# Performance work log

Measured on AMD Instinct MI355X. Metric: run time of the kernel, lower is better.

The kernel has to match this reference:

```python
import jax, jax.numpy as jnp
import numpy as np

EPS = 1e-7  # dummy-column epsilon from stanza utils.add_dummy(eps=True)


def setup_inputs() -> dict:
    key = jax.random.key(0)
    ks = jax.random.split(key, 9)
    n_mentions, emb = 10000, 1024
    batch, n_ants, pw_emb = 1024, 64, 64
    hidden = 1024
    in_features = 3 * emb + pw_emb  # 3136
    return {
        "all_mentions": jax.random.normal(ks[0], (n_mentions, emb), jnp.float32),
        "mentions_batch": jax.random.normal(ks[1], (batch, emb), jnp.float32),
        "pw_batch": jax.random.normal(ks[2], (batch, n_ants, pw_emb), jnp.float32),
        "top_indices_batch": jax.random.randint(ks[3], (batch, n_ants), 0, n_mentions),
        "top_rough_scores_batch": jax.random.normal(ks[4], (batch, n_ants), jnp.float32),
        "W1": jax.random.normal(ks[5], (hidden, in_features), jnp.float32) * 0.02,
        "b1": jax.random.normal(ks[6], (hidden,), jnp.float32) * 0.02,
        "Wout": jax.random.normal(ks[7], (1, hidden), jnp.float32) * 0.02,
        "bout": jax.random.normal(ks[8], (1,), jnp.float32) * 0.02,
    }


def reference(all_mentions, mentions_batch, pw_batch, top_indices_batch,
              top_rough_scores_batch, W1, b1, Wout, bout):
    n_ants = pw_batch.shape[1]
    # pair matrix: [batch, n_ants, 3*emb + pw_emb]
    a = jnp.broadcast_to(mentions_batch[:, None, :],
                         (mentions_batch.shape[0], n_ants, mentions_batch.shape[1]))
    b = all_mentions[top_indices_batch]          # gather: [batch, n_ants, emb]
    pair = jnp.concatenate((a, b, a * b, pw_batch), axis=2)
    # FFNN: Linear -> LeakyReLU (dropout is identity at eval) -> Linear(->1)
    h = jax.nn.leaky_relu(jnp.einsum('bnf,hf->bnh', pair, W1) + b1, negative_slope=0.01)
    ffnn = (jnp.einsum('bnh,oh->bno', h, Wout) + bout)[..., 0]  # [batch, n_ants]
    scores = top_rough_scores_batch + ffnn
    # add dummy column with eps at position 0 -> [batch, n_ants + 1]
    dummy = jnp.full((scores.shape[0], 1), EPS, scores.dtype)
    return jnp.concatenate((dummy, scores), axis=1)
```

## Files before the change

kernel.cpp:

```cpp
#include <hip/hip_runtime.h>
#include <hip/hip_bf16.h>
#include <cstdint>
#include <cstdio>

typedef unsigned short u16;
typedef unsigned int   u32;
typedef __attribute__((ext_vector_type(8))) short bf16x8;
typedef __attribute__((ext_vector_type(4))) float f32x4;
typedef __attribute__((ext_vector_type(4))) u16   u16x4;
typedef __attribute__((ext_vector_type(8))) u16   u16x8;

#define GLOBAL_AS __attribute__((address_space(1)))
#define LDS_AS    __attribute__((address_space(3)))

static __device__ __forceinline__ u16 f2bf(float f) {
  u32 u = __builtin_bit_cast(u32, f);
  u = (u + 0x7fffu + ((u >> 16) & 1u)) >> 16;
  return (u16)u;
}
static __device__ __forceinline__ float bf2f(u16 v) {
  return __builtin_bit_cast(float, (u32)v << 16);
}
static __device__ __forceinline__ void gload_lds16(const void* g, void* l) {
  __builtin_amdgcn_global_load_lds((GLOBAL_AS u32*)g, (LDS_AS u32*)l, 16, 0, 0);
}

__global__ void k_cvt(const float* __restrict__ src, int ld, int c0,
                      int rows_src, int cols4, int total4,
                      u16* __restrict__ dst, int ldd, int dcol) {
  int gid = blockIdx.x * 256 + threadIdx.x;
  if (gid >= total4) return;
  int r = gid / cols4;
  int c = (gid - r * cols4) * 4;
  u16x4 o = {0, 0, 0, 0};
  if (r < rows_src) {
    const float4 v = *(const float4*)&src[(size_t)r * ld + c0 + c];
    o[0] = f2bf(v.x); o[1] = f2bf(v.y); o[2] = f2bf(v.z); o[3] = f2bf(v.w);
  }
  *(u16x4*)&dst[(size_t)r * ldd + dcol + c] = o;
}

__global__ void k_init(const float* __restrict__ rough,
                       const float* __restrict__ bout,
                       float* __restrict__ out) {
  int i = blockIdx.x * 256 + threadIdx.x;
  if (i >= 1024 * 65) return;
  int bi = i / 65, c = i - bi * 65;
  out[i] = (c == 0) ? 1e-7f : rough[bi * 64 + c - 1] + bout[0];
}

__global__ void k_build_cmat(const u16* __restrict__ A16,
                             const u16* __restrict__ allm16,
                             const float* __restrict__ pw,
                             const int* __restrict__ topidx,
                             u16* __restrict__ Cmat, int r0) {
  int gid = blockIdx.x * 256 + threadIdx.x;
  int lr = gid / 136;
  int c8 = gid - lr * 136;
  int r  = r0 + lr;
  u16x8 o;
  if (c8 < 128) {
    int k   = c8 * 8;
    int idx = topidx[r];
    int bi  = r >> 6;
    u16x8 a = *(const u16x8*)&A16[(size_t)bi * 1024 + k];
    u16x8 b = *(const u16x8*)&allm16[(size_t)idx * 1024 + k];
#pragma unroll
    for (int j = 0; j < 8; ++j) o[j] = f2bf(bf2f(a[j]) * bf2f(b[j]));
  } else {
    int k = (c8 - 128) * 8;
    float4 p0 = *(const float4*)&pw[(size_t)r * 64 + k];
    float4 p1 = *(const float4*)&pw[(size_t)r * 64 + k + 4];
    o[0] = f2bf(p0.x); o[1] = f2bf(p0.y); o[2] = f2bf(p0.z); o[3] = f2bf(p0.w);
    o[4] = f2bf(p1.x); o[5] = f2bf(p1.y); o[6] = f2bf(p1.z); o[7] = f2bf(p1.w);
  }
  *(u16x8*)&Cmat[(size_t)lr * 1088 + c8 * 8] = o;
}

__global__ __launch_bounds__(256)
void gemm128(const u16* __restrict__ A, int lda,
             const u16* __restrict__ B, int ldb, int Ksteps,
             u16* __restrict__ C, int ldc, const float* __restrict__ bias) {
  __shared__ u16 As[128 * 64];
  __shared__ u16 Bs[128 * 64];
  const int t = threadIdx.x;
  const int w = t >> 6, l = t & 63;
  const int wr = w >> 1, wc = w & 1;
  const int brow = blockIdx.x * 128;
  const int bcol = blockIdx.y * 128;
  const int srow = t >> 3;
  const int scol = (t & 7) * 8;
  const int gsw  = (((t & 7) ^ ((t >> 3) & 7))) * 8;

  f32x4 acc[4][4] = {};
  for (int ks = 0; ks < Ksteps; ++ks) {
    const int kb = ks * 64;
#pragma unroll
    for (int q = 0; q < 4; ++q) {
      int r = q * 32 + srow;
      gload_lds16(A + (size_t)(brow + r) * lda + kb + gsw, &As[r * 64 + scol]);
      gload_lds16(B + (size_t)(bcol + r) * ldb + kb + gsw, &Bs[r * 64 + scol]);
    }
    __syncthreads();
#pragma unroll
    for (int kk = 0; kk < 2; ++kk) {
      bf16x8 af[4], bfr[4];
      const int pg = ((kk * 4 + (l >> 4)) ^ (l & 7)) * 8;
#pragma unroll
      for (int m = 0; m < 4; ++m)
        af[m] = *(const bf16x8*)&As[(wr * 64 + m * 16 + (l & 15)) * 64 + pg];
#pragma unroll
      for (int n = 0; n < 4; ++n)
        bfr[n] = *(const bf16x8*)&Bs[(wc * 64 + n * 16 + (l & 15)) * 64 + pg];
#pragma unroll
      for (int m = 0; m < 4; ++m)
#pragma unroll
        for (int n = 0; n < 4; ++n)
          acc[m][n] = __builtin_amdgcn_mfma_f32_16x16x32_bf16(af[m], bfr[n], acc[m][n], 0, 0, 0);
    }
    __syncthreads();
  }
#pragma unroll
  for (int m = 0; m < 4; ++m)
#pragma unroll
    for (int n = 0; n < 4; ++n)
#pragma unroll
      for (int reg = 0; reg < 4; ++reg) {
        int row = brow + wr * 64 + m * 16 + (l >> 4) * 4 + reg;
        int col = bcol + wc * 64 + n * 16 + (l & 15);
        float v = acc[m][n][reg] + (bias ? bias[col] : 0.f);
        C[(size_t)row * ldc + col] = f2bf(v);
      }
}

template<bool FUSED>
__global__ __launch_bounds__(512, 1)
void gemm256(const u16* __restrict__ A, int lda,
             const u16* __restrict__ B, int ldb, int NT,
             u16* __restrict__ C, int ldc,
             const u16* __restrict__ Aproj, const u16* __restrict__ Bproj,
             const float* __restrict__ Wout,
             const int* __restrict__ topidx, float* __restrict__ out, int r0) {
  extern __shared__ u16 lds[];
  u16* As = lds;
  u16* Bs = lds + 2 * 2 * 128 * 64;

  const int t = threadIdx.x;
  const int l = t & 63;
  const int w = t >> 6;
  const int wrow = w >> 2, wcol = w & 3;
  const int brow = blockIdx.x * 256;
  const int bcol = blockIdx.y * 256;

  const int sr  = t >> 3;
  const int sc  = (t & 7) * 8;
  const int gsw = ((t & 7) ^ (sr & 7)) * 8;

  auto stageA = [&](int kt, int h) {
    if (kt >= NT) return;
#pragma unroll
    for (int s = 0; s < 2; ++s) {
      int lr = sr + 64 * s;
      int g  = ((lr >> 5) << 6) + h * 32 + (lr & 31);
      gload_lds16(A + (size_t)(brow + g) * lda + kt * 64 + gsw,
                  &As[(((kt & 1) * 2 + h) * 128 + lr) * 64 + sc]);
    }
  };
  auto stageB = [&](int kt, int h) {
    if (kt >= NT) return;
#pragma unroll
    for (int s = 0; s < 2; ++s) {
      int lr = h * 128 + sr + 64 * s;
      gload_lds16(B + (size_t)(bcol + lr) * ldb + kt * 64 + gsw,
                  &Bs[((kt & 1) * 256 + lr) * 64 + sc]);
    }
  };

  f32x4 acc[8][4] = {};

  stageB(0, 0); stageB(0, 1); stageA(0, 0); stageA(0, 1);
  stageB(1, 0); stageB(1, 1);
  asm volatile("s_waitcnt vmcnt(6)" ::: "memory");
  __builtin_amdgcn_s_barrier();

  for (int kt = 0; kt < NT; ++kt) {
    const int cbuf = kt & 1;
    bf16x8 bfr[4][2];
#pragma unroll
    for (int q = 0; q < 4; ++q) {
      if (q == 0) {
#pragma unroll
        for (int n = 0; n < 4; ++n) {
          int row = wcol * 64 + n * 16 + (l & 15);
#pragma unroll
          for (int kk = 0; kk < 2; ++kk) {
            int gran = (kk * 4 + (l >> 4)) ^ (l & 7);
            bfr[n][kk] = *(const bf16x8*)&Bs[(cbuf * 256 + row) * 64 + gran * 8];
          }
        }
      }
      bf16x8 af[2][2];
#pragma unroll
      for (int m2 = 0; m2 < 2; ++m2) {
        int m = 2 * q + m2;
        int g = wrow * 128 + m * 16 + (l & 15);
        int lra = ((g >> 6) << 5) + (g & 31);
#pragma unroll
        for (int kk = 0; kk < 2; ++kk) {
          int gran = (kk * 4 + (l >> 4)) ^ (l & 7);
          af[m2][kk] = *(const bf16x8*)&As[((cbuf * 2 + (q & 1)) * 128 + lra) * 64 + gran * 8];
        }
      }

      if      (q == 0) stageA(kt + 1, 0);
      else if (q == 1) stageA(kt + 1, 1);
      else if (q == 2) stageB(kt + 2, 0);
      else             stageB(kt + 2, 1);

      if (q == 0) asm volatile("s_waitcnt lgkmcnt(8)" ::: "memory");
      __builtin_amdgcn_s_barrier();
      asm volatile("s_waitcnt lgkmcnt(0)" ::: "memory");
      __builtin_amdgcn_sched_barrier(0);
      __builtin_amdgcn_s_setprio(1);
#pragma unroll
      for (int m2 = 0; m2 < 2; ++m2)
#pragma unroll
        for (int n = 0; n < 4; ++n)
#pragma unroll
          for (int kk = 0; kk < 2; ++kk)
            acc[2 * q + m2][n] = __builtin_amdgcn_mfma_f32_16x16x32_bf16(
                af[m2][kk], bfr[n][kk], acc[2 * q + m2][n], 0, 0, 0);
      __builtin_amdgcn_s_setprio(0);

      if (q == 0) {
        if (kt + 1 < NT) asm volatile("s_waitcnt vmcnt(6)" ::: "memory");
        else             asm volatile("s_waitcnt vmcnt(0)" ::: "memory");
      } else if (q == 3 && kt + 1 < NT) {
        if (kt + 2 < NT) asm volatile("s_waitcnt vmcnt(6)" ::: "memory");
        else             asm volatile("s_waitcnt vmcnt(2)" ::: "memory");
      }
      __builtin_amdgcn_s_barrier();
    }
  }

  if constexpr (FUSED) {
    __syncthreads();
    u16* Pb = lds;
#pragma unroll
    for (int pass = 0; pass < 16; ++pass) {
      int rr = pass * 16 + (t >> 5);
      int mi = topidx[r0 + brow + rr];
      int cc = (t & 31) * 8;
      gload_lds16(&Bproj[(size_t)mi * 1024 + bcol + cc], &Pb[rr * 256 + cc]);
    }
    asm volatile("s_waitcnt vmcnt(0)" ::: "memory");
    __syncthreads();

    float wo[4], av[2][4];
    const int bi0 = ((r0 + brow) >> 6) + wrow * 2;
#pragma unroll
    for (int n = 0; n < 4; ++n) {
      int col = bcol + wcol * 64 + n * 16 + (l & 15);
      wo[n] = Wout[col];
#pragma unroll
      for (int j = 0; j < 2; ++j)
        av[j][n] = bf2f(Aproj[(size_t)(bi0 + j) * 1024 + col]);
    }
#pragma unroll
    for (int m = 0; m < 8; ++m) {
#pragma unroll
      for (int reg = 0; reg < 4; ++reg) {
        int lrow = wrow * 128 + m * 16 + (l >> 4) * 4 + reg;
        int gr = r0 + brow + lrow;
        float s = 0.f;
#pragma unroll
        for (int n = 0; n < 4; ++n) {
          int lcol = wcol * 64 + n * 16 + (l & 15);
          float v = acc[m][n][reg] + av[m >> 2][n] + bf2f(Pb[lrow * 256 + lcol]);
          v = v > 0.f ? v : 0.01f * v;
          s += v * wo[n];
        }
        s += __shfl_xor(s, 1);
        s += __shfl_xor(s, 2);
        s += __shfl_xor(s, 4);
        s += __shfl_xor(s, 8);
        if ((l & 15) == 0)
          atomicAdd(&out[(gr >> 6) * 65 + 1 + (gr & 63)], s);
      }
    }
  } else {
#pragma unroll
    for (int m = 0; m < 8; ++m)
#pragma unroll
      for (int n = 0; n < 4; ++n)
#pragma unroll
        for (int reg = 0; reg < 4; ++reg) {
          int row = brow + wrow * 128 + m * 16 + (l >> 4) * 4 + reg;
          int col = bcol + wcol * 64 + n * 16 + (l & 15);
          C[(size_t)row * ldc + col] = f2bf(acc[m][n][reg]);
        }
  }
}

extern "C" void kernel_launch(void* const* d_in, const int* in_sizes, int n_in,
                              void* d_out, int out_size, void* d_ws, size_t ws_size,
                              hipStream_t stream) {
  const float* allm  = (const float*)d_in[0];
  const float* ments = (const float*)d_in[1];
  const float* pw    = (const float*)d_in[2];
  const int*   tidx  = (const int*)d_in[3];
  const float* rough = (const float*)d_in[4];
  const float* W1    = (const float*)d_in[5];
  const float* b1    = (const float*)d_in[6];
  const float* Wout  = (const float*)d_in[7];
  const float* bout  = (const float*)d_in[8];
  float* out = (float*)d_out;

  const int CHUNK = 16384;
  u16* A16    = (u16*)d_ws;
  u16* allm16 = A16 + 1024 * 1024;
  u16* W1a    = allm16 + 10240 * 1024;
  u16* W1b    = W1a + 1024 * 1024;
  u16* W1cp   = W1b + 1024 * 1024;
  u16* Aproj  = W1cp + 1024 * 1088;
  u16* Bproj  = Aproj + 1024 * 1024;
  u16* Cmat   = Bproj + 10240 * 1024;

  size_t need = (size_t)2 * ((size_t)1024*1024 + 10240*1024 + 1024*1024 + 1024*1024
              + 1024*1088 + 1024*1024 + 10240*1024 + (size_t)CHUNK*1088);
  if (ws_size < need) {
    fprintf(stderr, "kernel_launch: ws_size %zu < needed %zu\n", ws_size, need);
    return;
  }

  hipFuncSetAttribute((const void*)&gemm256<false>,
                      hipFuncAttributeMaxDynamicSharedMemorySize, 131072);
  hipFuncSetAttribute((const void*)&gemm256<true>,
                      hipFuncAttributeMaxDynamicSharedMemorySize, 131072);

  {
    int t4;
    t4 = 1024 * 256;
    k_cvt<<<(t4 + 255) / 256, 256, 0, stream>>>(W1, 3136, 0,    1024, 256, t4, W1a, 1024, 0);
    k_cvt<<<(t4 + 255) / 256, 256, 0, stream>>>(W1, 3136, 1024, 1024, 256, t4, W1b, 1024, 0);
    k_cvt<<<(t4 + 255) / 256, 256, 0, stream>>>(W1, 3136, 2048, 1024, 256, t4, W1cp, 1088, 0);
    t4 = 1024 * 16;
    k_cvt<<<(t4 + 255) / 256, 256, 0, stream>>>(W1, 3136, 3072, 1024, 16, t4, W1cp, 1088, 1024);
    t4 = 1024 * 256;
    k_cvt<<<(t4 + 255) / 256, 256, 0, stream>>>(ments, 1024, 0, 1024, 256, t4, A16, 1024, 0);
    t4 = 10240 * 256;
    k_cvt<<<(t4 + 255) / 256, 256, 0, stream>>>(allm, 1024, 0, 10000, 256, t4, allm16, 1024, 0);
  }

  gemm128<<<dim3(8, 8), 256, 0, stream>>>(A16, 1024, W1a, 1024, 16, Aproj, 1024, b1);
  gemm256<false><<<dim3(40, 4), 512, 131072, stream>>>(allm16, 1024, W1b, 1024, 16,
                                                       Bproj, 1024,
                                                       nullptr, nullptr, nullptr,
                                                       nullptr, nullptr, 0);

  k_init<<<260, 256, 0, stream>>>(rough, bout, out);

  for (int c = 0; c < 4; ++c) {
    int r0 = c * CHUNK;
    k_build_cmat<<<(CHUNK * 136) / 256, 256, 0, stream>>>(A16, allm16, pw, tidx, Cmat, r0);
    gemm256<true><<<dim3(CHUNK / 256, 4), 512, 131072, stream>>>(Cmat, 1088, W1cp, 1088, 17,
                                                                 nullptr, 0,
                                                                 Aproj, Bproj, Wout,
                                                                 tidx, out, r0);
  }
}
```

Measured before the change: 319.9 us.

## Fuse pair-matrix construction into fused GEMM A-tile staging, drop Cmat chunks

Removes the separate k_build_cmat kernel and its intermediate Cmat buffer. The fused GEMM now gathers mention rows and all_mentions rows by index, multiplies them, and converts pw to bf16 in registers before writing the A tile into LDS, pipelined across K steps. The four chunked launches become a single launch over all rows, and the Bproj epilogue tile gets an XOR swizzle to reduce LDS bank conflicts. In exchange, A staging moves from async global-to-LDS loads to register loads plus VALU work, and the waitcnt scheduling is reworked. This can stall the MFMA pipeline and raise register pressure.

```diff
diff --git a/kernel.cpp b/kernel.cpp
--- a/kernel.cpp
+++ b/kernel.cpp
@@ -47,34 +47,6 @@
   if (i >= 1024 * 65) return;
   int bi = i / 65, c = i - bi * 65;
   out[i] = (c == 0) ? 1e-7f : rough[bi * 64 + c - 1] + bout[0];
-}
-
-__global__ void k_build_cmat(const u16* __restrict__ A16,
-                             const u16* __restrict__ allm16,
-                             const float* __restrict__ pw,
-                             const int* __restrict__ topidx,
-                             u16* __restrict__ Cmat, int r0) {
-  int gid = blockIdx.x * 256 + threadIdx.x;
-  int lr = gid / 136;
-  int c8 = gid - lr * 136;
-  int r  = r0 + lr;
-  u16x8 o;
-  if (c8 < 128) {
-    int k   = c8 * 8;
-    int idx = topidx[r];
-    int bi  = r >> 6;
-    u16x8 a = *(const u16x8*)&A16[(size_t)bi * 1024 + k];
-    u16x8 b = *(const u16x8*)&allm16[(size_t)idx * 1024 + k];
-#pragma unroll
-    for (int j = 0; j < 8; ++j) o[j] = f2bf(bf2f(a[j]) * bf2f(b[j]));
-  } else {
-    int k = (c8 - 128) * 8;
-    float4 p0 = *(const float4*)&pw[(size_t)r * 64 + k];
-    float4 p1 = *(const float4*)&pw[(size_t)r * 64 + k + 4];
-    o[0] = f2bf(p0.x); o[1] = f2bf(p0.y); o[2] = f2bf(p0.z); o[3] = f2bf(p0.w);
-    o[4] = f2bf(p1.x); o[5] = f2bf(p1.y); o[6] = f2bf(p1.z); o[7] = f2bf(p1.w);
-  }
-  *(u16x8*)&Cmat[(size_t)lr * 1088 + c8 * 8] = o;
 }
 
 __global__ __launch_bounds__(256)
@@ -138,9 +110,11 @@
 void gemm256(const u16* __restrict__ A, int lda,
              const u16* __restrict__ B, int ldb, int NT,
              u16* __restrict__ C, int ldc,
+             const u16* __restrict__ a16, const u16* __restrict__ allm16,
+             const float* __restrict__ pw,
              const u16* __restrict__ Aproj, const u16* __restrict__ Bproj,
              const float* __restrict__ Wout,
-             const int* __restrict__ topidx, float* __restrict__ out, int r0) {
+             const int* __restrict__ topidx, float* __restrict__ out) {
   extern __shared__ u16 lds[];
   u16* As = lds;
   u16* Bs = lds + 2 * 2 * 128 * 64;
@@ -156,6 +130,20 @@
   const int sc  = (t & 7) * 8;
   const int gsw = ((t & 7) ^ (sr & 7)) * 8;
 
+  int mi_[2][2], bi_[2][2], grow_[2][2];
+  if constexpr (FUSED) {
+#pragma unroll
+    for (int h = 0; h < 2; ++h)
+#pragma unroll
+      for (int s = 0; s < 2; ++s) {
+        int lr = sr + 64 * s;
+        int g  = ((lr >> 5) << 6) + h * 32 + (lr & 31);
+        grow_[h][s] = brow + g;
+        mi_[h][s]   = topidx[brow + g];
+        bi_[h][s]   = (brow + g) >> 6;
+      }
+  }
+
   auto stageA = [&](int kt, int h) {
     if (kt >= NT) return;
 #pragma unroll
@@ -175,17 +163,66 @@
                   &Bs[((kt & 1) * 256 + lr) * 64 + sc]);
     }
   };
+  auto issueG = [&](int kt1, int h, u16x8* ga, u16x8* gb, float4 (*gp)[2]) {
+    if (kt1 >= NT) return;
+#pragma unroll
+    for (int s = 0; s < 2; ++s) {
+      int lr  = sr + 64 * s;
+      int swc = sc ^ ((lr & 7) << 3);
+      if (kt1 == NT - 1) {
+        const float* p = &pw[(size_t)grow_[h][s] * 64 + swc];
+        gp[s][0] = *(const float4*)p;
+        gp[s][1] = *(const float4*)(p + 4);
+      } else {
+        int col = kt1 * 64 + swc;
+        ga[s] = *(const u16x8*)&a16[(size_t)bi_[h][s] * 1024 + col];
+        gb[s] = *(const u16x8*)&allm16[(size_t)mi_[h][s] * 1024 + col];
+      }
+    }
+  };
+  auto writeA = [&](int kt1, int h, u16x8* ga, u16x8* gb, float4 (*gp)[2]) {
+    if (kt1 >= NT) return;
+#pragma unroll
+    for (int s = 0; s < 2; ++s) {
+      int lr = sr + 64 * s;
+      u16x8 o;
+      if (kt1 == NT - 1) {
+        o[0] = f2bf(gp[s][0].x); o[1] = f2bf(gp[s][0].y);
+        o[2] = f2bf(gp[s][0].z); o[3] = f2bf(gp[s][0].w);
+        o[4] = f2bf(gp[s][1].x); o[5] = f2bf(gp[s][1].y);
+        o[6] = f2bf(gp[s][1].z); o[7] = f2bf(gp[s][1].w);
+      } else {
+#pragma unroll
+        for (int j = 0; j < 8; ++j) o[j] = f2bf(bf2f(ga[s][j]) * bf2f(gb[s][j]));
+      }
+      *(u16x8*)&As[(((kt1 & 1) * 2 + h) * 128 + lr) * 64 + sc] = o;
+    }
+  };
 
   f32x4 acc[8][4] = {};
 
-  stageB(0, 0); stageB(0, 1); stageA(0, 0); stageA(0, 1);
-  stageB(1, 0); stageB(1, 1);
-  asm volatile("s_waitcnt vmcnt(6)" ::: "memory");
+  if constexpr (FUSED) {
+    u16x8 pga0[2], pgb0[2], pga1[2], pgb1[2];
+    float4 pgp0[2][2], pgp1[2][2];
+    issueG(0, 0, pga0, pgb0, pgp0);
+    issueG(0, 1, pga1, pgb1, pgp1);
+    stageB(0, 0); stageB(0, 1); stageB(1, 0); stageB(1, 1);
+    writeA(0, 0, pga0, pgb0, pgp0);
+    writeA(0, 1, pga1, pgb1, pgp1);
+    asm volatile("s_waitcnt lgkmcnt(0)" ::: "memory");
+    asm volatile("s_waitcnt vmcnt(4)" ::: "memory");
+  } else {
+    stageB(0, 0); stageB(0, 1); stageA(0, 0); stageA(0, 1);
+    stageB(1, 0); stageB(1, 1);
+    asm volatile("s_waitcnt vmcnt(6)" ::: "memory");
+  }
   __builtin_amdgcn_s_barrier();
 
   for (int kt = 0; kt < NT; ++kt) {
     const int cbuf = kt & 1;
     bf16x8 bfr[4][2];
+    u16x8 ga0[2], gb0[2], ga1[2], gb1[2];
+    float4 gp0[2][2], gp1[2][2];
 #pragma unroll
     for (int q = 0; q < 4; ++q) {
       if (q == 0) {
@@ -212,10 +249,25 @@
         }
       }
 
-      if      (q == 0) stageA(kt + 1, 0);
-      else if (q == 1) stageA(kt + 1, 1);
-      else if (q == 2) stageB(kt + 2, 0);
-      else             stageB(kt + 2, 1);
+      if constexpr (FUSED) {
+        if (q == 1) {
+          issueG(kt + 1, 0, ga0, gb0, gp0);
+        } else if (q == 2) {
+          writeA(kt + 1, 0, ga0, gb0, gp0);
+          issueG(kt + 1, 1, ga1, gb1, gp1);
+          stageB(kt + 2, 0);
+          asm volatile("s_waitcnt lgkmcnt(0)" ::: "memory");
+        } else if (q == 3) {
+          writeA(kt + 1, 1, ga1, gb1, gp1);
+          stageB(kt + 2, 1);
+          asm volatile("s_waitcnt lgkmcnt(0)" ::: "memory");
+        }
+      } else {
+        if      (q == 0) stageA(kt + 1, 0);
+        else if (q == 1) stageA(kt + 1, 1);
+        else if (q == 2) stageB(kt + 2, 0);
+        else             stageB(kt + 2, 1);
+      }
 
       if (q == 0) asm volatile("s_waitcnt lgkmcnt(8)" ::: "memory");
       __builtin_amdgcn_s_barrier();
@@ -232,12 +284,14 @@
                 af[m2][kk], bfr[n][kk], acc[2 * q + m2][n], 0, 0, 0);
       __builtin_amdgcn_s_setprio(0);
 
-      if (q == 0) {
-        if (kt + 1 < NT) asm volatile("s_waitcnt vmcnt(6)" ::: "memory");
-        else             asm volatile("s_waitcnt vmcnt(0)" ::: "memory");
-      } else if (q == 3 && kt + 1 < NT) {
-        if (kt + 2 < NT) asm volatile("s_waitcnt vmcnt(6)" ::: "memory");
-        else             asm volatile("s_waitcnt vmcnt(2)" ::: "memory");
+      if constexpr (!FUSED) {
+        if (q == 0) {
+          if (kt + 1 < NT) asm volatile("s_waitcnt vmcnt(6)" ::: "memory");
+          else             asm volatile("s_waitcnt vmcnt(0)" ::: "memory");
+        } else if (q == 3 && kt + 1 < NT) {
+          if (kt + 2 < NT) asm volatile("s_waitcnt vmcnt(6)" ::: "memory");
+          else             asm volatile("s_waitcnt vmcnt(2)" ::: "memory");
+        }
       }
       __builtin_amdgcn_s_barrier();
     }
@@ -249,15 +303,16 @@
 #pragma unroll
     for (int pass = 0; pass < 16; ++pass) {
       int rr = pass * 16 + (t >> 5);
-      int mi = topidx[r0 + brow + rr];
+      int mi = topidx[brow + rr];
       int cc = (t & 31) * 8;
-      gload_lds16(&Bproj[(size_t)mi * 1024 + bcol + cc], &Pb[rr * 256 + cc]);
+      int scc = cc ^ (((rr >> 1) & 7) << 3);
+      gload_lds16(&Bproj[(size_t)mi * 1024 + bcol + scc], &Pb[rr * 256 + cc]);
     }
     asm volatile("s_waitcnt vmcnt(0)" ::: "memory");
     __syncthreads();
 
     float wo[4], av[2][4];
-    const int bi0 = ((r0 + brow) >> 6) + wrow * 2;
+    const int bi0 = (brow >> 6) + wrow * 2;
 #pragma unroll
     for (int n = 0; n < 4; ++n) {
       int col = bcol + wcol * 64 + n * 16 + (l & 15);
@@ -271,12 +326,13 @@
 #pragma unroll
       for (int reg = 0; reg < 4; ++reg) {
         int lrow = wrow * 128 + m * 16 + (l >> 4) * 4 + reg;
-        int gr = r0 + brow + lrow;
+        int gr = brow + lrow;
+        int key = ((lrow >> 1) & 7) << 3;
         float s = 0.f;
 #pragma unroll
         for (int n = 0; n < 4; ++n) {
           int lcol = wcol * 64 + n * 16 + (l & 15);
-          float v = acc[m][n][reg] + av[m >> 2][n] + bf2f(Pb[lrow * 256 + lcol]);
+          float v = acc[m][n][reg] + av[m >> 2][n] + bf2f(Pb[lrow * 256 + (lcol ^ key)]);
           v = v > 0.f ? v : 0.01f * v;
           s += v * wo[n];
         }
@@ -316,7 +372,6 @@
   const float* bout  = (const float*)d_in[8];
   float* out = (float*)d_out;
 
-  const int CHUNK = 16384;
   u16* A16    = (u16*)d_ws;
   u16* allm16 = A16 + 1024 * 1024;
   u16* W1a    = allm16 + 10240 * 1024;
@@ -324,10 +379,9 @@
   u16* W1cp   = W1b + 1024 * 1024;
   u16* Aproj  = W1cp + 1024 * 1088;
   u16* Bproj  = Aproj + 1024 * 1024;
-  u16* Cmat   = Bproj + 10240 * 1024;
 
   size_t need = (size_t)2 * ((size_t)1024*1024 + 10240*1024 + 1024*1024 + 1024*1024
-              + 1024*1088 + 1024*1024 + 10240*1024 + (size_t)CHUNK*1088);
+              + 1024*1088 + 1024*1024 + 10240*1024);
   if (ws_size < need) {
     fprintf(stderr, "kernel_launch: ws_size %zu < needed %zu\n", ws_size, need);
     return;
@@ -356,16 +410,14 @@
   gemm256<false><<<dim3(40, 4), 512, 131072, stream>>>(allm16, 1024, W1b, 1024, 16,
                                                        Bproj, 1024,
                                                        nullptr, nullptr, nullptr,
-                                                       nullptr, nullptr, 0);
+                                                       nullptr, nullptr, nullptr,
+                                                       nullptr, nullptr);
 
   k_init<<<260, 256, 0, stream>>>(rough, bout, out);
 
-  for (int c = 0; c < 4; ++c) {
-    int r0 = c * CHUNK;
-    k_build_cmat<<<(CHUNK * 136) / 256, 256, 0, stream>>>(A16, allm16, pw, tidx, Cmat, r0);
-    gemm256<true><<<dim3(CHUNK / 256, 4), 512, 131072, stream>>>(Cmat, 1088, W1cp, 1088, 17,
-                                                                 nullptr, 0,
-                                                                 Aproj, Bproj, Wout,
-                                                                 tidx, out, r0);
-  }
-}
+  gemm256<true><<<dim3(256, 4), 512, 131072, stream>>>(nullptr, 0, W1cp, 1088, 17,
+                                                       nullptr, 0,
+                                                       A16, allm16, pw,
+                                                       Aproj, Bproj, Wout,
+                                                       tidx, out);
+}
```

Result: slower. 700.2 us (+118.9%).

## Replace 256x256 fused main GEMM with 128x128 two-blocks-per-CU fused kernel

Applied to the files above, without the earlier changes.

The fused pair-score GEMM moves from a 256x256-tile, 512-thread, one-block-per-CU kernel to a 128x128-tile, 256-thread kernel with static LDS and launch bounds allowing two blocks per CU. It also gets a finer-grained staging pipeline and an XOR-swizzled LDS layout for the gathered Bproj epilogue. The goal is better occupancy, overlap between resident blocks and fewer epilogue bank conflicts. The cost is less operand reuse per tile, more total global and LDS traffic, and twice as many atomicAdds to the output.

```diff
diff --git a/kernel.cpp b/kernel.cpp
--- a/kernel.cpp
+++ b/kernel.cpp
@@ -133,14 +133,10 @@
       }
 }
 
-template<bool FUSED>
 __global__ __launch_bounds__(512, 1)
-void gemm256(const u16* __restrict__ A, int lda,
-             const u16* __restrict__ B, int ldb, int NT,
-             u16* __restrict__ C, int ldc,
-             const u16* __restrict__ Aproj, const u16* __restrict__ Bproj,
-             const float* __restrict__ Wout,
-             const int* __restrict__ topidx, float* __restrict__ out, int r0) {
+void gemm256p(const u16* __restrict__ A, int lda,
+              const u16* __restrict__ B, int ldb, int NT,
+              u16* __restrict__ C, int ldc) {
   extern __shared__ u16 lds[];
   u16* As = lds;
   u16* Bs = lds + 2 * 2 * 128 * 64;
@@ -151,7 +147,6 @@
   const int wrow = w >> 2, wcol = w & 3;
   const int brow = blockIdx.x * 256;
   const int bcol = blockIdx.y * 256;
-
   const int sr  = t >> 3;
   const int sc  = (t & 7) * 8;
   const int gsw = ((t & 7) ^ (sr & 7)) * 8;
@@ -177,7 +172,6 @@
   };
 
   f32x4 acc[8][4] = {};
-
   stageB(0, 0); stageB(0, 1); stageA(0, 0); stageA(0, 1);
   stageB(1, 0); stageB(1, 1);
   asm volatile("s_waitcnt vmcnt(6)" ::: "memory");
@@ -243,62 +237,163 @@
     }
   }
 
-  if constexpr (FUSED) {
-    __syncthreads();
-    u16* Pb = lds;
-#pragma unroll
-    for (int pass = 0; pass < 16; ++pass) {
-      int rr = pass * 16 + (t >> 5);
-      int mi = topidx[r0 + brow + rr];
-      int cc = (t & 31) * 8;
-      gload_lds16(&Bproj[(size_t)mi * 1024 + bcol + cc], &Pb[rr * 256 + cc]);
-    }
-    asm volatile("s_waitcnt vmcnt(0)" ::: "memory");
-    __syncthreads();
-
-    float wo[4], av[2][4];
-    const int bi0 = ((r0 + brow) >> 6) + wrow * 2;
-#pragma unroll
-    for (int n = 0; n < 4; ++n) {
-      int col = bcol + wcol * 64 + n * 16 + (l & 15);
-      wo[n] = Wout[col];
-#pragma unroll
-      for (int j = 0; j < 2; ++j)
-        av[j][n] = bf2f(Aproj[(size_t)(bi0 + j) * 1024 + col]);
-    }
-#pragma unroll
-    for (int m = 0; m < 8; ++m) {
+#pragma unroll
+  for (int m = 0; m < 8; ++m)
+#pragma unroll
+    for (int n = 0; n < 4; ++n)
 #pragma unroll
       for (int reg = 0; reg < 4; ++reg) {
-        int lrow = wrow * 128 + m * 16 + (l >> 4) * 4 + reg;
-        int gr = r0 + brow + lrow;
-        float s = 0.f;
+        int row = brow + wrow * 128 + m * 16 + (l >> 4) * 4 + reg;
+        int col = bcol + wcol * 64 + n * 16 + (l & 15);
+        C[(size_t)row * ldc + col] = f2bf(acc[m][n][reg]);
+      }
+}
+
+__global__ __launch_bounds__(256, 2)
+void gemm128f(const u16* __restrict__ A, int lda,
+              const u16* __restrict__ B, int ldb, int NT,
+              const u16* __restrict__ Aproj, const u16* __restrict__ Bproj,
+              const float* __restrict__ Wout,
+              const int* __restrict__ topidx, float* __restrict__ out, int r0) {
+  __shared__ u16 As[2][128][64];
+  __shared__ u16 Bs[2][128][64];
+
+  const int t = threadIdx.x;
+  const int l = t & 63;
+  const int w = t >> 6;
+  const int wr = w >> 1, wc = w & 1;
+  const int brow = blockIdx.x * 128;
+  const int bcol = blockIdx.y * 128;
+
+  const int sr  = t >> 3;
+  const int sc  = (t & 7) * 8;
+  const int gsw = ((t & 7) ^ (sr & 7)) * 8;
+
+  auto stageBh = [&](int kt, int h) {
+    if (kt >= NT) return;
+    const int nb = kt & 1;
+#pragma unroll
+    for (int s = 0; s < 2; ++s) {
+      int row = h * 64 + s * 32 + sr;
+      gload_lds16(B + (size_t)(bcol + row) * ldb + kt * 64 + gsw,
+                  &Bs[nb][row][sc]);
+    }
+  };
+  auto stageAp = [&](int kt, int p) {
+    if (kt >= NT) return;
+    const int nb = kt & 1;
+#pragma unroll
+    for (int s = 0; s < 2; ++s) {
+      int row = (p + s * 2) * 32 + sr;
+      gload_lds16(A + (size_t)(brow + row) * lda + kt * 64 + gsw,
+                  &As[nb][row][sc]);
+    }
+  };
+
+  f32x4 acc[4][4] = {};
+
+  stageBh(0, 0); stageBh(0, 1); stageAp(0, 0); stageAp(0, 1);
+  asm volatile("s_waitcnt vmcnt(2)" ::: "memory");
+  __builtin_amdgcn_s_barrier();
+
+  for (int kt = 0; kt < NT; ++kt) {
+    const int buf = kt & 1;
+    const bool hn = (kt + 1 < NT);
+    bf16x8 bfr[4][2];
+#pragma unroll
+    for (int q = 0; q < 4; ++q) {
+      if (q == 0) {
 #pragma unroll
         for (int n = 0; n < 4; ++n) {
-          int lcol = wcol * 64 + n * 16 + (l & 15);
-          float v = acc[m][n][reg] + av[m >> 2][n] + bf2f(Pb[lrow * 256 + lcol]);
-          v = v > 0.f ? v : 0.01f * v;
-          s += v * wo[n];
+          int row = wc * 64 + n * 16 + (l & 15);
+#pragma unroll
+          for (int kk = 0; kk < 2; ++kk) {
+            int gran = (kk * 4 + (l >> 4)) ^ (l & 7);
+            bfr[n][kk] = *(const bf16x8*)&Bs[buf][row][gran * 8];
+          }
         }
-        s += __shfl_xor(s, 1);
-        s += __shfl_xor(s, 2);
-        s += __shfl_xor(s, 4);
-        s += __shfl_xor(s, 8);
-        if ((l & 15) == 0)
-          atomicAdd(&out[(gr >> 6) * 65 + 1 + (gr & 63)], s);
-      }
-    }
-  } else {
-#pragma unroll
-    for (int m = 0; m < 8; ++m)
+      }
+      bf16x8 af[2];
+      {
+        int row = wr * 64 + q * 16 + (l & 15);
+#pragma unroll
+        for (int kk = 0; kk < 2; ++kk) {
+          int gran = (kk * 4 + (l >> 4)) ^ (l & 7);
+          af[kk] = *(const bf16x8*)&As[buf][row][gran * 8];
+        }
+      }
+
+      if      (q == 0) stageBh(kt + 1, 0);
+      else if (q == 1) stageBh(kt + 1, 1);
+      else if (q == 2) stageAp(kt + 1, 0);
+      else             stageAp(kt + 1, 1);
+
+      __builtin_amdgcn_s_barrier();
+      asm volatile("s_waitcnt lgkmcnt(0)" ::: "memory");
+      __builtin_amdgcn_sched_barrier(0);
+      __builtin_amdgcn_s_setprio(1);
 #pragma unroll
       for (int n = 0; n < 4; ++n)
 #pragma unroll
-        for (int reg = 0; reg < 4; ++reg) {
-          int row = brow + wrow * 128 + m * 16 + (l >> 4) * 4 + reg;
-          int col = bcol + wcol * 64 + n * 16 + (l & 15);
-          C[(size_t)row * ldc + col] = f2bf(acc[m][n][reg]);
-        }
+        for (int kk = 0; kk < 2; ++kk)
+          acc[q][n] = __builtin_amdgcn_mfma_f32_16x16x32_bf16(
+              af[kk], bfr[n][kk], acc[q][n], 0, 0, 0);
+      __builtin_amdgcn_s_setprio(0);
+
+      if (q == 1) {
+        if (hn) asm volatile("s_waitcnt vmcnt(4)" ::: "memory");
+        else    asm volatile("s_waitcnt vmcnt(0)" ::: "memory");
+      } else if (q == 3 && hn) {
+        asm volatile("s_waitcnt vmcnt(2)" ::: "memory");
+      }
+      __builtin_amdgcn_s_barrier();
+    }
+  }
+
+  __syncthreads();
+  u16* Pb = &As[0][0][0];
+#pragma unroll
+  for (int pass = 0; pass < 8; ++pass) {
+    int rr = pass * 16 + (t >> 4);
+    int mi = topidx[r0 + brow + rr];
+    int cc = (t & 15) * 8;
+    int scc = cc ^ (((rr >> 2) & 3) << 4);
+    gload_lds16(&Bproj[(size_t)mi * 1024 + bcol + scc], &Pb[rr * 128 + cc]);
+  }
+  asm volatile("s_waitcnt vmcnt(0)" ::: "memory");
+  __syncthreads();
+
+  float wo[4], av[2][4];
+  const int bi0 = ((r0 + brow) >> 6) + wr;
+#pragma unroll
+  for (int n = 0; n < 4; ++n) {
+    int col = bcol + wc * 64 + n * 16 + (l & 15);
+    wo[n] = Wout[col];
+    av[0][n] = bf2f(Aproj[(size_t)bi0 * 1024 + col]);
+    av[1][n] = av[0][n];
+  }
+#pragma unroll
+  for (int m = 0; m < 4; ++m) {
+#pragma unroll
+    for (int reg = 0; reg < 4; ++reg) {
+      int lrow = wr * 64 + m * 16 + (l >> 4) * 4 + reg;
+      int gr = r0 + brow + lrow;
+      int key = ((lrow >> 2) & 3) << 4;
+      float s = 0.f;
+#pragma unroll
+      for (int n = 0; n < 4; ++n) {
+        int lcol = wc * 64 + n * 16 + (l & 15);
+        float v = acc[m][n][reg] + av[0][n] + bf2f(Pb[lrow * 128 + (lcol ^ key)]);
+        v = v > 0.f ? v : 0.01f * v;
+        s += v * wo[n];
+      }
+      s += __shfl_xor(s, 1);
+      s += __shfl_xor(s, 2);
+      s += __shfl_xor(s, 4);
+      s += __shfl_xor(s, 8);
+      if ((l & 15) == 0)
+        atomicAdd(&out[(gr >> 6) * 65 + 1 + (gr & 63)], s);
+    }
   }
 }
 
@@ -333,9 +428,7 @@
     return;
   }
 
-  hipFuncSetAttribute((const void*)&gemm256<false>,
-                      hipFuncAttributeMaxDynamicSharedMemorySize, 131072);
-  hipFuncSetAttribute((const void*)&gemm256<true>,
+  hipFuncSetAttribute((const void*)&gemm256p,
                       hipFuncAttributeMaxDynamicSharedMemorySize, 131072);
 
   {
@@ -353,19 +446,14 @@
   }
 
   gemm128<<<dim3(8, 8), 256, 0, stream>>>(A16, 1024, W1a, 1024, 16, Aproj, 1024, b1);
-  gemm256<false><<<dim3(40, 4), 512, 131072, stream>>>(allm16, 1024, W1b, 1024, 16,
-                                                       Bproj, 1024,
-                                                       nullptr, nullptr, nullptr,
-                                                       nullptr, nullptr, 0);
+  gemm256p<<<dim3(40, 4), 512, 131072, stream>>>(allm16, 1024, W1b, 1024, 16, Bproj, 1024);
 
   k_init<<<260, 256, 0, stream>>>(rough, bout, out);
 
   for (int c = 0; c < 4; ++c) {
     int r0 = c * CHUNK;
     k_build_cmat<<<(CHUNK * 136) / 256, 256, 0, stream>>>(A16, allm16, pw, tidx, Cmat, r0);
-    gemm256<true><<<dim3(CHUNK / 256, 4), 512, 131072, stream>>>(Cmat, 1088, W1cp, 1088, 17,
-                                                                 nullptr, 0,
-                                                                 Aproj, Bproj, Wout,
-                                                                 tidx, out, r0);
-  }
-}
+    gemm128f<<<dim3(CHUNK / 128, 8), 256, 0, stream>>>(Cmat, 1088, W1cp, 1088, 17,
+                                                       Aproj, Bproj, Wout, tidx, out, r0);
+  }
+}
```

New measurement: 388.6 us. 1.21x slower.

## Overlap gathered Bproj epilogue loads with final GEMM K-iteration

Applied to the files above, without the earlier changes.

The gather of projected B rows for the fused epilogue is split into two 128-column halves. The first half is issued into the freed B buffer during the last K-tile's MFMA phases, and the second half goes into the A buffer after the loop, so the gather latency overlaps compute instead of following a full sync. Gather indices are prefetched into registers at kernel start, and the LDS layout uses an XOR swizzle to reduce bank conflicts in the epilogue reads. This adds register pressure from the eight index registers and brings in subtle buffer-reuse hazards on the last iteration.

```diff
diff --git a/kernel.cpp b/kernel.cpp
--- a/kernel.cpp
+++ b/kernel.cpp
@@ -156,6 +156,14 @@
   const int sc  = (t & 7) * 8;
   const int gsw = ((t & 7) ^ (sr & 7)) * 8;
 
+  int mi_pb[8];
+  if constexpr (FUSED) {
+#pragma unroll
+    for (int p = 0; p < 8; ++p)
+      mi_pb[p] = topidx[r0 + brow + p * 32 + (t >> 4)];
+    asm volatile("s_waitcnt vmcnt(0)" ::: "memory");
+  }
+
   auto stageA = [&](int kt, int h) {
     if (kt >= NT) return;
 #pragma unroll
@@ -175,6 +183,19 @@
                   &Bs[((kt & 1) * 256 + lr) * 64 + sc]);
     }
   };
+  auto stagePb = [&](int half, int p0, int np) {
+    u16* dst = half ? As : Bs;
+#pragma unroll
+    for (int pi = 0; pi < 3; ++pi) {
+      if (pi >= np) break;
+      int p  = p0 + pi;
+      int rr = p * 32 + (t >> 4);
+      int cc = (t & 15) * 8;
+      int key = ((rr >> 2) & 3) << 4;
+      gload_lds16(&Bproj[(size_t)mi_pb[p] * 1024 + bcol + half * 128 + (cc ^ key)],
+                  &dst[rr * 128 + cc]);
+    }
+  };
 
   f32x4 acc[8][4] = {};
 
@@ -185,6 +206,7 @@
 
   for (int kt = 0; kt < NT; ++kt) {
     const int cbuf = kt & 1;
+    const bool lastT = (kt + 1 >= NT);
     bf16x8 bfr[4][2];
 #pragma unroll
     for (int q = 0; q < 4; ++q) {
@@ -212,10 +234,18 @@
         }
       }
 
-      if      (q == 0) stageA(kt + 1, 0);
-      else if (q == 1) stageA(kt + 1, 1);
-      else if (q == 2) stageB(kt + 2, 0);
-      else             stageB(kt + 2, 1);
+      if (q == 0) {
+        stageA(kt + 1, 0);
+      } else if (q == 1) {
+        if (!lastT) stageA(kt + 1, 1);
+        else if (FUSED) stagePb(0, 0, 3);
+      } else if (q == 2) {
+        if (kt + 2 < NT) stageB(kt + 2, 0);
+        else if (lastT && FUSED) stagePb(0, 3, 3);
+      } else {
+        if (kt + 2 < NT) stageB(kt + 2, 1);
+        else if (lastT && FUSED) stagePb(0, 6, 2);
+      }
 
       if (q == 0) asm volatile("s_waitcnt lgkmcnt(8)" ::: "memory");
       __builtin_amdgcn_s_barrier();
@@ -233,9 +263,9 @@
       __builtin_amdgcn_s_setprio(0);
 
       if (q == 0) {
-        if (kt + 1 < NT) asm volatile("s_waitcnt vmcnt(6)" ::: "memory");
-        else             asm volatile("s_waitcnt vmcnt(0)" ::: "memory");
-      } else if (q == 3 && kt + 1 < NT) {
+        if (!lastT) asm volatile("s_waitcnt vmcnt(6)" ::: "memory");
+        else        asm volatile("s_waitcnt vmcnt(0)" ::: "memory");
+      } else if (q == 3 && !lastT) {
         if (kt + 2 < NT) asm volatile("s_waitcnt vmcnt(6)" ::: "memory");
         else             asm volatile("s_waitcnt vmcnt(2)" ::: "memory");
       }
@@ -244,17 +274,12 @@
   }
 
   if constexpr (FUSED) {
-    __syncthreads();
-    u16* Pb = lds;
-#pragma unroll
-    for (int pass = 0; pass < 16; ++pass) {
-      int rr = pass * 16 + (t >> 5);
-      int mi = topidx[r0 + brow + rr];
-      int cc = (t & 31) * 8;
-      gload_lds16(&Bproj[(size_t)mi * 1024 + bcol + cc], &Pb[rr * 256 + cc]);
-    }
+    stagePb(1, 0, 3); stagePb(1, 3, 3); stagePb(1, 6, 2);
     asm volatile("s_waitcnt vmcnt(0)" ::: "memory");
     __syncthreads();
+
+    const u16* PbLo = Bs;
+    const u16* PbHi = As;
 
     float wo[4], av[2][4];
     const int bi0 = ((r0 + brow) >> 6) + wrow * 2;
@@ -266,17 +291,20 @@
       for (int j = 0; j < 2; ++j)
         av[j][n] = bf2f(Aproj[(size_t)(bi0 + j) * 1024 + col]);
     }
+    const u16* Pb = (wcol < 2) ? PbLo : PbHi;
+    const int colBase = (wcol & 1) * 64;
 #pragma unroll
     for (int m = 0; m < 8; ++m) {
 #pragma unroll
       for (int reg = 0; reg < 4; ++reg) {
         int lrow = wrow * 128 + m * 16 + (l >> 4) * 4 + reg;
         int gr = r0 + brow + lrow;
+        int key = ((lrow >> 2) & 3) << 4;
         float s = 0.f;
 #pragma unroll
         for (int n = 0; n < 4; ++n) {
-          int lcol = wcol * 64 + n * 16 + (l & 15);
-          float v = acc[m][n][reg] + av[m >> 2][n] + bf2f(Pb[lrow * 256 + lcol]);
+          int hcol = colBase + n * 16 + (l & 15);
+          float v = acc[m][n][reg] + av[m >> 2][n] + bf2f(Pb[lrow * 128 + (hcol ^ key)]);
           v = v > 0.f ? v : 0.01f * v;
           s += v * wo[n];
         }
```

Result: slower. 329.4 us (+3.0%).
